# Performance work log

Measured on AMD Instinct MI355X. Metric: run time of the kernel, lower is better.

Reference implementation:

```python
import jax, jax.numpy as jnp
import numpy as np

# per-position segment id for seq_len=16: slices [0:1],[1:6],[6:9],[9:10],[10:16]
SEG = np.array([0] + [1]*5 + [2]*3 + [3] + [4]*6, dtype=np.int32)
HEAD_DIM = 3
NUM_HEADS = 2


def setup_inputs() -> dict:
    key = jax.random.key(0)
    ks = jax.random.split(key, 9)
    B = 262144
    s = 1.0 / np.sqrt(6.0)  # torch Linear init scale
    return {
        "x": jax.random.normal(ks[0], (B, 16, 6), dtype=jnp.float32),
        "Wq": jax.random.uniform(ks[1], (5, 6, 6), jnp.float32, -s, s),
        "bq": jax.random.uniform(ks[2], (5, 6), jnp.float32, -s, s),
        "Wk": jax.random.uniform(ks[3], (5, 6, 6), jnp.float32, -s, s),
        "bk": jax.random.uniform(ks[4], (5, 6), jnp.float32, -s, s),
        "Wv": jax.random.uniform(ks[5], (5, 6, 6), jnp.float32, -s, s),
        "bv": jax.random.uniform(ks[6], (5, 6), jnp.float32, -s, s),
        "Wo": jax.random.uniform(ks[7], (6, 6), jnp.float32, -s, s),
        "bo": jax.random.uniform(ks[8], (6,), jnp.float32, -s, s),
    }


def reference(x, Wq, bq, Wk, bk, Wv, bv, Wo, bo):
    B, S, D = x.shape  # S=16, D=6
    seg = jnp.asarray(SEG)

    def seg_proj(W, b):
        # torch Linear: y = x @ W.T + b; gather per-position segment weights
        return jnp.einsum('bsd,sod->bso', x, W[seg]) + b[seg]

    def heads(t):
        return t.reshape(B, S, NUM_HEADS, HEAD_DIM).transpose(0, 2, 1, 3)

    Q = heads(seg_proj(Wq, bq))  # [B,H,S,hd]
    K = heads(seg_proj(Wk, bk))
    V = heads(seg_proj(Wv, bv))

    scores = jnp.einsum('bhqd,bhkd->bhqk', Q, K) / jnp.sqrt(jnp.float32(HEAD_DIM))
    attn = jax.nn.softmax(scores, axis=-1)
    ctx = jnp.einsum('bhqk,bhkd->bhqd', attn, V)
    ctx = ctx.transpose(0, 2, 1, 3).reshape(B, S, D)
    return ctx @ Wo.T + bo
```

## Files before the change

kernel.cpp:

```cpp
#include <hip/hip_runtime.h>

#define QSCALE 0.83294038f

#define WAVE_FLOATS 1056
#define VOFF 528
#define GSTRIDE 132

__device__ __forceinline__ void proj6(const float* __restrict__ W5,
                                      const float* __restrict__ b5,
                                      int seg,
                                      float x0, float x1, float x2,
                                      float x3, float x4, float x5,
                                      float r[6])
{
    float w[36];
    const float4* p = (const float4*)(W5 + seg * 36);
    #pragma unroll
    for (int i = 0; i < 9; ++i) {
        float4 v = p[i];
        w[i*4+0] = v.x; w[i*4+1] = v.y; w[i*4+2] = v.z; w[i*4+3] = v.w;
    }
    float bb[6];
    const float2* bp = (const float2*)(b5 + seg * 6);
    #pragma unroll
    for (int i = 0; i < 3; ++i) { float2 v = bp[i]; bb[i*2] = v.x; bb[i*2+1] = v.y; }
    #pragma unroll
    for (int j = 0; j < 6; ++j) {
        r[j] = bb[j] + x0*w[j*6+0] + x1*w[j*6+1] + x2*w[j*6+2]
                     + x3*w[j*6+3] + x4*w[j*6+4] + x5*w[j*6+5];
    }
}

__global__ __launch_bounds__(256) void attn_seg_kernel(
    const float* __restrict__ x,
    const float* __restrict__ Wq, const float* __restrict__ bq,
    const float* __restrict__ Wk, const float* __restrict__ bk,
    const float* __restrict__ Wv, const float* __restrict__ bv,
    const float* __restrict__ Wo, const float* __restrict__ bo,
    float* __restrict__ out, int total)
{
    __shared__ __align__(16) float lds[4 * WAVE_FLOATS];
    const int t    = threadIdx.x;
    const int wv_  = t >> 6;
    const int g    = (t >> 4) & 3;
    const int s    = t & 15;

    const int seg = (s == 0) ? 0 : (s < 6) ? 1 : (s < 9) ? 2 : (s == 9) ? 3 : 4;

    const int pos = blockIdx.x * 256 + t;
    const bool valid = pos < total;
    float x0=0.f,x1=0.f,x2=0.f,x3=0.f,x4=0.f,x5=0.f;
    if (valid) {
        const float* xp = x + (size_t)pos * 6;
        float2 a = *(const float2*)(xp);
        float2 b = *(const float2*)(xp + 2);
        float2 c = *(const float2*)(xp + 4);
        x0=a.x; x1=a.y; x2=b.x; x3=b.y; x4=c.x; x5=c.y;
    }

    float q[6], kk[6], vvv[6];
    proj6(Wq, bq, seg, x0,x1,x2,x3,x4,x5, q);
    proj6(Wk, bk, seg, x0,x1,x2,x3,x4,x5, kk);
    proj6(Wv, bv, seg, x0,x1,x2,x3,x4,x5, vvv);
    #pragma unroll
    for (int i = 0; i < 6; ++i) q[i] *= QSCALE;

    float* Kd = &lds[wv_ * WAVE_FLOATS + g * GSTRIDE + s * 8];
    *(float4*)Kd       = make_float4(kk[0], kk[1], kk[2], kk[3]);
    *(float2*)(Kd + 4) = make_float2(kk[4], kk[5]);
    float* Vd = Kd + VOFF;
    *(float4*)Vd       = make_float4(vvv[0], vvv[1], vvv[2], vvv[3]);
    *(float2*)(Vd + 4) = make_float2(vvv[4], vvv[5]);

    __builtin_amdgcn_wave_barrier();
    asm volatile("s_waitcnt lgkmcnt(0)" ::: "memory");
    __builtin_amdgcn_sched_barrier(0);

    const float* Kb = &lds[wv_ * WAVE_FLOATS + g * GSTRIDE];
    const float* Vb = Kb + VOFF;
    float s0 = 0.f, s1 = 0.f;
    float c0=0.f,c1=0.f,c2=0.f,c3=0.f,c4=0.f,c5=0.f;
    #pragma unroll
    for (int k = 0; k < 16; ++k) {
        float4 ka = *(const float4*)(Kb + k * 8);
        float2 kb = *(const float2*)(Kb + k * 8 + 4);
        float e0 = __builtin_amdgcn_exp2f(q[0]*ka.x + q[1]*ka.y + q[2]*ka.z);
        float e1 = __builtin_amdgcn_exp2f(q[3]*ka.w + q[4]*kb.x + q[5]*kb.y);
        float4 va = *(const float4*)(Vb + k * 8);
        float2 vb = *(const float2*)(Vb + k * 8 + 4);
        s0 += e0; s1 += e1;
        c0 += e0*va.x; c1 += e0*va.y; c2 += e0*va.z;
        c3 += e1*va.w; c4 += e1*vb.x; c5 += e1*vb.y;
    }
    const float i0 = __builtin_amdgcn_rcpf(s0);
    const float i1 = __builtin_amdgcn_rcpf(s1);
    c0 *= i0; c1 *= i0; c2 *= i0;
    c3 *= i1; c4 *= i1; c5 *= i1;

    float o_[6];
    #pragma unroll
    for (int i = 0; i < 6; ++i) {
        o_[i] = bo[i] + c0*Wo[i*6+0] + c1*Wo[i*6+1] + c2*Wo[i*6+2]
                      + c3*Wo[i*6+3] + c4*Wo[i*6+4] + c5*Wo[i*6+5];
    }

    if (valid) {
        float* op = out + (size_t)pos * 6;
        *(float2*)(op)     = make_float2(o_[0], o_[1]);
        *(float2*)(op + 2) = make_float2(o_[2], o_[3]);
        *(float2*)(op + 4) = make_float2(o_[4], o_[5]);
    }
}

extern "C" void kernel_launch(void* const* d_in, const int* in_sizes, int n_in,
                              void* d_out, int out_size, void* d_ws, size_t ws_size,
                              hipStream_t stream) {
    const float* x  = (const float*)d_in[0];
    const float* Wq = (const float*)d_in[1];
    const float* bq = (const float*)d_in[2];
    const float* Wk = (const float*)d_in[3];
    const float* bk = (const float*)d_in[4];
    const float* Wv = (const float*)d_in[5];
    const float* bv = (const float*)d_in[6];
    const float* Wo = (const float*)d_in[7];
    const float* bo = (const float*)d_in[8];
    float* out = (float*)d_out;

    const int total = in_sizes[0] / 6;
    const int grid  = (total + 255) / 256;
    attn_seg_kernel<<<grid, 256, 0, stream>>>(x, Wq, bq, Wk, bk, Wv, bv, Wo, bo, out, total);
}
```

Baseline: 250.1 us.

## Use persistent grid-stride blocks with x prefetch and interleaved K/V LDS layout

Grid is capped at 2048 blocks, each looping over tiles with a grid stride. The next tile's x values are prefetched into registers while the current tile computes, to hide global load latency. K and V are packed into one 12-float record per position so each key needs three float4 LDS reads, and per-segment weight pointers are hoisted out of the loop behind asm barriers to keep them per-lane. The risks are higher register pressure from the prefetch and fewer blocks, which may cut latency hiding through occupancy.

```diff
diff --git a/kernel.cpp b/kernel.cpp
--- a/kernel.cpp
+++ b/kernel.cpp
@@ -2,28 +2,26 @@
 
 #define QSCALE 0.83294038f
 
-#define WAVE_FLOATS 1056
-#define VOFF 528
-#define GSTRIDE 132
+#define GSTRIDE 196
+#define WAVE_FLOATS 784
+#define MAXBLOCKS 2048
 
-__device__ __forceinline__ void proj6(const float* __restrict__ W5,
-                                      const float* __restrict__ b5,
-                                      int seg,
+__device__ __forceinline__ void proj6(const float* wp, const float* bp,
                                       float x0, float x1, float x2,
                                       float x3, float x4, float x5,
                                       float r[6])
 {
     float w[36];
-    const float4* p = (const float4*)(W5 + seg * 36);
+    const float4* p = (const float4*)wp;
     #pragma unroll
     for (int i = 0; i < 9; ++i) {
         float4 v = p[i];
         w[i*4+0] = v.x; w[i*4+1] = v.y; w[i*4+2] = v.z; w[i*4+3] = v.w;
     }
     float bb[6];
-    const float2* bp = (const float2*)(b5 + seg * 6);
+    const float2* b2 = (const float2*)bp;
     #pragma unroll
-    for (int i = 0; i < 3; ++i) { float2 v = bp[i]; bb[i*2] = v.x; bb[i*2+1] = v.y; }
+    for (int i = 0; i < 3; ++i) { float2 v = b2[i]; bb[i*2] = v.x; bb[i*2+1] = v.y; }
     #pragma unroll
     for (int j = 0; j < 6; ++j) {
         r[j] = bb[j] + x0*w[j*6+0] + x1*w[j*6+1] + x2*w[j*6+2]
@@ -40,75 +38,117 @@
     float* __restrict__ out, int total)
 {
     __shared__ __align__(16) float lds[4 * WAVE_FLOATS];
-    const int t    = threadIdx.x;
-    const int wv_  = t >> 6;
-    const int g    = (t >> 4) & 3;
-    const int s    = t & 15;
-
+    const int t   = threadIdx.x;
+    const int wv_ = t >> 6;
+    const int g   = (t >> 4) & 3;
+    const int s   = t & 15;
     const int seg = (s == 0) ? 0 : (s < 6) ? 1 : (s < 9) ? 2 : (s == 9) ? 3 : 4;
 
-    const int pos = blockIdx.x * 256 + t;
-    const bool valid = pos < total;
+    float* const kvg = &lds[wv_ * WAVE_FLOATS + g * GSTRIDE];
+    float* const kvw = kvg + s * 12;
+
+    const float* const wqb = Wq + seg * 36;
+    const float* const wkb = Wk + seg * 36;
+    const float* const wvb = Wv + seg * 36;
+    const float* const bqb = bq + seg * 6;
+    const float* const bkb = bk + seg * 6;
+    const float* const bvb = bv + seg * 6;
+
+    const int ntiles = (total + 255) >> 8;
+
+    int tile = blockIdx.x;
     float x0=0.f,x1=0.f,x2=0.f,x3=0.f,x4=0.f,x5=0.f;
-    if (valid) {
-        const float* xp = x + (size_t)pos * 6;
-        float2 a = *(const float2*)(xp);
-        float2 b = *(const float2*)(xp + 2);
-        float2 c = *(const float2*)(xp + 4);
-        x0=a.x; x1=a.y; x2=b.x; x3=b.y; x4=c.x; x5=c.y;
+    {
+        const int pos = (tile << 8) + t;
+        if (pos < total) {
+            const float* xp = x + (size_t)pos * 6;
+            float2 a = *(const float2*)(xp);
+            float2 b = *(const float2*)(xp + 2);
+            float2 c = *(const float2*)(xp + 4);
+            x0=a.x; x1=a.y; x2=b.x; x3=b.y; x4=c.x; x5=c.y;
+        }
     }
 
-    float q[6], kk[6], vvv[6];
-    proj6(Wq, bq, seg, x0,x1,x2,x3,x4,x5, q);
-    proj6(Wk, bk, seg, x0,x1,x2,x3,x4,x5, kk);
-    proj6(Wv, bv, seg, x0,x1,x2,x3,x4,x5, vvv);
-    #pragma unroll
-    for (int i = 0; i < 6; ++i) q[i] *= QSCALE;
+    #pragma unroll 1
+    for (; tile < ntiles; ) {
+        const int pos   = (tile << 8) + t;
+        const bool valid = pos < total;
+        const int ntile = tile + gridDim.x;
 
-    float* Kd = &lds[wv_ * WAVE_FLOATS + g * GSTRIDE + s * 8];
-    *(float4*)Kd       = make_float4(kk[0], kk[1], kk[2], kk[3]);
-    *(float2*)(Kd + 4) = make_float2(kk[4], kk[5]);
-    float* Vd = Kd + VOFF;
-    *(float4*)Vd       = make_float4(vvv[0], vvv[1], vvv[2], vvv[3]);
-    *(float2*)(Vd + 4) = make_float2(vvv[4], vvv[5]);
+        float nx0=0.f,nx1=0.f,nx2=0.f,nx3=0.f,nx4=0.f,nx5=0.f;
+        if (ntile < ntiles) {
+            const int npos = (ntile << 8) + t;
+            if (npos < total) {
+                const float* xp = x + (size_t)npos * 6;
+                float2 a = *(const float2*)(xp);
+                float2 b = *(const float2*)(xp + 2);
+                float2 c = *(const float2*)(xp + 4);
+                nx0=a.x; nx1=a.y; nx2=b.x; nx3=b.y; nx4=c.x; nx5=c.y;
+            }
+        }
 
-    __builtin_amdgcn_wave_barrier();
-    asm volatile("s_waitcnt lgkmcnt(0)" ::: "memory");
-    __builtin_amdgcn_sched_barrier(0);
+        float kk[6], vvv[6], q[6];
+        {
+            const float* wp = wkb; const float* bp = bkb;
+            asm volatile("" : "+v"(wp), "+v"(bp));
+            proj6(wp, bp, x0,x1,x2,x3,x4,x5, kk);
+        }
+        {
+            const float* wp = wvb; const float* bp = bvb;
+            asm volatile("" : "+v"(wp), "+v"(bp));
+            proj6(wp, bp, x0,x1,x2,x3,x4,x5, vvv);
+        }
+        {
+            const float* wp = wqb; const float* bp = bqb;
+            asm volatile("" : "+v"(wp), "+v"(bp));
+            proj6(wp, bp, x0,x1,x2,x3,x4,x5, q);
+        }
+        #pragma unroll
+        for (int i = 0; i < 6; ++i) q[i] *= QSCALE;
 
-    const float* Kb = &lds[wv_ * WAVE_FLOATS + g * GSTRIDE];
-    const float* Vb = Kb + VOFF;
-    float s0 = 0.f, s1 = 0.f;
-    float c0=0.f,c1=0.f,c2=0.f,c3=0.f,c4=0.f,c5=0.f;
-    #pragma unroll
-    for (int k = 0; k < 16; ++k) {
-        float4 ka = *(const float4*)(Kb + k * 8);
-        float2 kb = *(const float2*)(Kb + k * 8 + 4);
-        float e0 = __builtin_amdgcn_exp2f(q[0]*ka.x + q[1]*ka.y + q[2]*ka.z);
-        float e1 = __builtin_amdgcn_exp2f(q[3]*ka.w + q[4]*kb.x + q[5]*kb.y);
-        float4 va = *(const float4*)(Vb + k * 8);
-        float2 vb = *(const float2*)(Vb + k * 8 + 4);
-        s0 += e0; s1 += e1;
-        c0 += e0*va.x; c1 += e0*va.y; c2 += e0*va.z;
-        c3 += e1*va.w; c4 += e1*vb.x; c5 += e1*vb.y;
-    }
-    const float i0 = __builtin_amdgcn_rcpf(s0);
-    const float i1 = __builtin_amdgcn_rcpf(s1);
-    c0 *= i0; c1 *= i0; c2 *= i0;
-    c3 *= i1; c4 *= i1; c5 *= i1;
+        *(float4*)(kvw)     = make_float4(kk[0], kk[1], kk[2], kk[3]);
+        *(float4*)(kvw + 4) = make_float4(kk[4], kk[5], vvv[0], vvv[1]);
+        *(float4*)(kvw + 8) = make_float4(vvv[2], vvv[3], vvv[4], vvv[5]);
 
-    float o_[6];
-    #pragma unroll
-    for (int i = 0; i < 6; ++i) {
-        o_[i] = bo[i] + c0*Wo[i*6+0] + c1*Wo[i*6+1] + c2*Wo[i*6+2]
-                      + c3*Wo[i*6+3] + c4*Wo[i*6+4] + c5*Wo[i*6+5];
-    }
+        __builtin_amdgcn_wave_barrier();
+        asm volatile("s_waitcnt lgkmcnt(0)" ::: "memory");
+        __builtin_amdgcn_sched_barrier(0);
 
-    if (valid) {
-        float* op = out + (size_t)pos * 6;
-        *(float2*)(op)     = make_float2(o_[0], o_[1]);
-        *(float2*)(op + 2) = make_float2(o_[2], o_[3]);
-        *(float2*)(op + 4) = make_float2(o_[4], o_[5]);
+        float s0 = 0.f, s1 = 0.f;
+        float c0=0.f,c1=0.f,c2=0.f,c3=0.f,c4=0.f,c5=0.f;
+        #pragma unroll
+        for (int k = 0; k < 16; ++k) {
+            float4 a = *(const float4*)(kvg + k * 12);
+            float4 b = *(const float4*)(kvg + k * 12 + 4);
+            float4 c = *(const float4*)(kvg + k * 12 + 8);
+            float e0 = __builtin_amdgcn_exp2f(q[0]*a.x + q[1]*a.y + q[2]*a.z);
+            float e1 = __builtin_amdgcn_exp2f(q[3]*a.w + q[4]*b.x + q[5]*b.y);
+            s0 += e0; s1 += e1;
+            c0 += e0*b.z; c1 += e0*b.w; c2 += e0*c.x;
+            c3 += e1*c.y; c4 += e1*c.z; c5 += e1*c.w;
+        }
+        const float i0 = __builtin_amdgcn_rcpf(s0);
+        const float i1 = __builtin_amdgcn_rcpf(s1);
+        c0 *= i0; c1 *= i0; c2 *= i0;
+        c3 *= i1; c4 *= i1; c5 *= i1;
+
+        float o_[6];
+        #pragma unroll
+        for (int i = 0; i < 6; ++i) {
+            o_[i] = bo[i] + c0*Wo[i*6+0] + c1*Wo[i*6+1] + c2*Wo[i*6+2]
+                          + c3*Wo[i*6+3] + c4*Wo[i*6+4] + c5*Wo[i*6+5];
+        }
+        if (valid) {
+            float* op = out + (size_t)pos * 6;
+            *(float2*)(op)     = make_float2(o_[0], o_[1]);
+            *(float2*)(op + 2) = make_float2(o_[2], o_[3]);
+            *(float2*)(op + 4) = make_float2(o_[4], o_[5]);
+        }
+
+        __builtin_amdgcn_wave_barrier();
+
+        x0=nx0; x1=nx1; x2=nx2; x3=nx3; x4=nx4; x5=nx5;
+        tile = ntile;
     }
 }
 
@@ -126,7 +166,8 @@
     const float* bo = (const float*)d_in[8];
     float* out = (float*)d_out;
 
-    const int total = in_sizes[0] / 6;
-    const int grid  = (total + 255) / 256;
+    const int total  = in_sizes[0] / 6;
+    const int ntiles = (total + 255) / 256;
+    const int grid   = ntiles < MAXBLOCKS ? ntiles : MAXBLOCKS;
     attn_seg_kernel<<<grid, 256, 0, stream>>>(x, Wq, bq, Wk, bk, Wv, bv, Wo, bo, out, total);
 }
```

After: 260.7 us. 4.2% more time.
